# Performance work log

Hardware: AMD Instinct MI355X
Metric: run time of the kernel (lower is better)

## Reference

```python
import jax, jax.numpy as jnp
import numpy as np

L = 512      # number of grid points
B = 32768    # batch of independent trajectories


def _rhs(y, w):
    # y: [4, B] -> dy: [4, B]; tiny coupled polynomial vector field
    A, T, N, C = y
    dA = w[0] + w[1] * A + w[2] * A ** 2
    dT = w[3] + w[4] * T + w[5] * T ** 2 + w[6] * A + w[7] * A ** 2 + w[8] * A * T
    dN = w[9] + w[10] * N + w[11] * N ** 2 + w[12] * T + w[13] * T ** 2 + w[14] * T * N
    dC = w[15] + w[16] * C + w[17] * C ** 2 + w[18] * N + w[19] * N ** 2 + w[20] * N * C
    return jnp.stack([dA, dT, dN, dC])


def setup_inputs() -> dict:
    key = jax.random.key(0)
    k1, k2 = jax.random.split(key)
    s_grid = jnp.arange(L, dtype=jnp.float32) * 0.01  # increasing grid, small h
    y0 = jax.random.normal(k1, (4, B), dtype=jnp.float32)
    w = jax.random.normal(k2, (21,), dtype=jnp.float32) * 0.001  # nn.Parameter init
    return {"s_grid": s_grid, "y0": y0, "w": w}


def reference(s_grid, y0, w):
    hs = jnp.diff(s_grid)  # [L-1] step sizes h_i = s[i] - s[i-1]

    def step(y, h):
        y_next = y + h * _rhs(y, w)  # explicit Euler
        return y_next, y_next

    _, ys = jax.lax.scan(step, y0, hs)          # [L-1, 4, B]
    return jnp.concatenate([y0[None], ys], 0)   # [L, 4, B]
```

## Files before the change

### kernel.cpp

```cpp
#include <hip/hip_runtime.h>


#define ODE_L 512
#define ODE_B 32768
#define G     8

#define ODE_STEP(h)                                                          \
  do {                                                                       \
    const float dA = w0  + w1  * A + w2  * A * A;                            \
    const float dT = w3  + w4  * T + w5  * T * T + w6  * A + w7  * A * A +   \
                     w8  * A * T;                                            \
    const float dN = w9  + w10 * N + w11 * N * N + w12 * T + w13 * T * T +   \
                     w14 * T * N;                                            \
    const float dC = w15 + w16 * C + w17 * C * C + w18 * N + w19 * N * N +   \
                     w20 * N * C;                                            \
    A += h * dA; T += h * dT; N += h * dN; C += h * dC;                      \
  } while (0)

#define ODE_GROUP(OFS, R0V)                                                  \
  do {                                                                       \
    _Pragma("unroll")                                                        \
    for (int j = 0; j < G; ++j) {                                            \
      const float h = sh_h[(R0V) + j - 1];                                   \
      ODE_STEP(h);                                                           \
      bA[(OFS) + j] = A; bT[(OFS) + j] = T;                                  \
      bN[(OFS) + j] = N; bC[(OFS) + j] = C;                                  \
    }                                                                        \
    _Pragma("unroll")                                                        \
    for (int j = 0; j < G; ++j) {                                            \
      const unsigned o = ((R0V) + j) * (4u * ODE_B) + b;                     \
      out[o + 0u * ODE_B] = bA[(OFS) + j];                                   \
      out[o + 1u * ODE_B] = bT[(OFS) + j];                                   \
      out[o + 2u * ODE_B] = bN[(OFS) + j];                                   \
      out[o + 3u * ODE_B] = bC[(OFS) + j];                                   \
    }                                                                        \
  } while (0)

__global__ __launch_bounds__(64) void population_ode_kernel(
    const float* __restrict__ s_grid,
    const float* __restrict__ y0,
    const float* __restrict__ w,
    float* __restrict__ out)
{
    __shared__ float sh_h[ODE_L - 1];

    const int tid = threadIdx.x;
    #pragma unroll
    for (int i = tid; i < ODE_L - 1; i += 64) {
        sh_h[i] = s_grid[i + 1] - s_grid[i];
    }

    const float w0  = w[0],  w1  = w[1],  w2  = w[2];
    const float w3  = w[3],  w4  = w[4],  w5  = w[5],  w6  = w[6],  w7 = w[7],
                w8  = w[8];
    const float w9  = w[9],  w10 = w[10], w11 = w[11], w12 = w[12],
                w13 = w[13], w14 = w[14];
    const float w15 = w[15], w16 = w[16], w17 = w[17], w18 = w[18],
                w19 = w[19], w20 = w[20];

    __syncthreads();

    const unsigned b = blockIdx.x * 64u + (unsigned)tid;

    float A = y0[0 * ODE_B + b];
    float T = y0[1 * ODE_B + b];
    float N = y0[2 * ODE_B + b];
    float C = y0[3 * ODE_B + b];

    out[0u * ODE_B + b] = A;
    out[1u * ODE_B + b] = T;
    out[2u * ODE_B + b] = N;
    out[3u * ODE_B + b] = C;

    float bA[2 * G], bT[2 * G], bN[2 * G], bC[2 * G];

    for (unsigned g = 0; g < 31; ++g) {
        const unsigned r0 = 1u + g * (2 * G);
        ODE_GROUP(0, r0);
        ODE_GROUP(G, r0 + G);
    }

    ODE_GROUP(0, 497u);

    #pragma unroll
    for (int j = 0; j < 7; ++j) {
        const float h = sh_h[504 + j];
        ODE_STEP(h);
        bA[G + j] = A; bT[G + j] = T; bN[G + j] = N; bC[G + j] = C;
    }
    #pragma unroll
    for (int j = 0; j < 7; ++j) {
        const unsigned o = (505u + j) * (4u * ODE_B) + b;
        out[o + 0u * ODE_B] = bA[G + j];
        out[o + 1u * ODE_B] = bT[G + j];
        out[o + 2u * ODE_B] = bN[G + j];
        out[o + 3u * ODE_B] = bC[G + j];
    }
}

extern "C" void kernel_launch(void* const* d_in, const int* in_sizes, int n_in,
                              void* d_out, int out_size, void* d_ws, size_t ws_size,
                              hipStream_t stream) {
    (void)in_sizes; (void)n_in; (void)d_ws; (void)ws_size; (void)out_size;

    const float* s_grid = (const float*)d_in[0];
    const float* y0     = (const float*)d_in[1];
    const float* w      = (const float*)d_in[2];
    float* out          = (float*)d_out;

    population_ode_kernel<<<dim3(ODE_B / 64), dim3(64), 0, stream>>>(
        s_grid, y0, w, out);
}
```

Measured before the change: 265.0 us.

## Warp-specialize: one compute wave feeds four store waves via double-buffered LDS

Splits each block into a compute wave that integrates the Euler steps and four store waves, each writing one state component, with results exchanged through a double-buffered LDS buffer and barriers per group of steps. The aim is to overlap the serial ODE arithmetic with the global output stores and increase memory-level parallelism. The trade-offs are a block-wide barrier every eight steps and larger blocks.

```diff
diff --git a/kernel.cpp b/kernel.cpp
--- a/kernel.cpp
+++ b/kernel.cpp
@@ -4,6 +4,8 @@
 #define ODE_L 512
 #define ODE_B 32768
 #define G     8
+#define NGRP  64
+#define TPB   320
 
 #define ODE_STEP(h)                                                          \
   do {                                                                       \
@@ -17,36 +19,25 @@
     A += h * dA; T += h * dT; N += h * dN; C += h * dC;                      \
   } while (0)
 
-#define ODE_GROUP(OFS, R0V)                                                  \
-  do {                                                                       \
-    _Pragma("unroll")                                                        \
-    for (int j = 0; j < G; ++j) {                                            \
-      const float h = sh_h[(R0V) + j - 1];                                   \
-      ODE_STEP(h);                                                           \
-      bA[(OFS) + j] = A; bT[(OFS) + j] = T;                                  \
-      bN[(OFS) + j] = N; bC[(OFS) + j] = C;                                  \
-    }                                                                        \
-    _Pragma("unroll")                                                        \
-    for (int j = 0; j < G; ++j) {                                            \
-      const unsigned o = ((R0V) + j) * (4u * ODE_B) + b;                     \
-      out[o + 0u * ODE_B] = bA[(OFS) + j];                                   \
-      out[o + 1u * ODE_B] = bT[(OFS) + j];                                   \
-      out[o + 2u * ODE_B] = bN[(OFS) + j];                                   \
-      out[o + 3u * ODE_B] = bC[(OFS) + j];                                   \
-    }                                                                        \
-  } while (0)
+__device__ __forceinline__ void sync_lds() {
+    asm volatile("s_waitcnt lgkmcnt(0)" ::: "memory");
+    __builtin_amdgcn_s_barrier();
+}
 
-__global__ __launch_bounds__(64) void population_ode_kernel(
+__global__ __launch_bounds__(TPB) void population_ode_kernel(
     const float* __restrict__ s_grid,
     const float* __restrict__ y0,
     const float* __restrict__ w,
     float* __restrict__ out)
 {
     __shared__ float sh_h[ODE_L - 1];
+    __shared__ float buf[2][G][4][64];
 
-    const int tid = threadIdx.x;
-    #pragma unroll
-    for (int i = tid; i < ODE_L - 1; i += 64) {
+    const int tid  = threadIdx.x;
+    const int wid  = tid >> 6;
+    const int lane = tid & 63;
+
+    for (int i = tid; i < ODE_L - 1; i += TPB) {
         sh_h[i] = s_grid[i + 1] - s_grid[i];
     }
 
@@ -58,43 +49,61 @@
     const float w15 = w[15], w16 = w[16], w17 = w[17], w18 = w[18],
                 w19 = w[19], w20 = w[20];
 
-    __syncthreads();
+    const unsigned b = blockIdx.x * 64u + (unsigned)lane;
 
-    const unsigned b = blockIdx.x * 64u + (unsigned)tid;
+    sync_lds();
 
-    float A = y0[0 * ODE_B + b];
-    float T = y0[1 * ODE_B + b];
-    float N = y0[2 * ODE_B + b];
-    float C = y0[3 * ODE_B + b];
+    if (wid == 0) {
+        float A = y0[0 * ODE_B + b];
+        float T = y0[1 * ODE_B + b];
+        float N = y0[2 * ODE_B + b];
+        float C = y0[3 * ODE_B + b];
 
-    out[0u * ODE_B + b] = A;
-    out[1u * ODE_B + b] = T;
-    out[2u * ODE_B + b] = N;
-    out[3u * ODE_B + b] = C;
+        for (unsigned g = 0; g < NGRP - 1; ++g) {
+            const int p = (int)(g & 1u);
+            #pragma unroll
+            for (int j = 0; j < G; ++j) {
+                const float h = sh_h[g * G + j];
+                ODE_STEP(h);
+                buf[p][j][0][lane] = A;
+                buf[p][j][1][lane] = T;
+                buf[p][j][2][lane] = N;
+                buf[p][j][3][lane] = C;
+            }
+            sync_lds();
+        }
+        #pragma unroll
+        for (int j = 0; j < 7; ++j) {
+            const float h = sh_h[504 + j];
+            ODE_STEP(h);
+            buf[1][j][0][lane] = A;
+            buf[1][j][1][lane] = T;
+            buf[1][j][2][lane] = N;
+            buf[1][j][3][lane] = C;
+        }
+        sync_lds();
+    } else {
+        const int st = wid - 1;
+        const unsigned ob = (unsigned)st * ODE_B + b;
 
-    float bA[2 * G], bT[2 * G], bN[2 * G], bC[2 * G];
+        out[ob] = y0[ob];
+        sync_lds();
 
-    for (unsigned g = 0; g < 31; ++g) {
-        const unsigned r0 = 1u + g * (2 * G);
-        ODE_GROUP(0, r0);
-        ODE_GROUP(G, r0 + G);
-    }
-
-    ODE_GROUP(0, 497u);
-
-    #pragma unroll
-    for (int j = 0; j < 7; ++j) {
-        const float h = sh_h[504 + j];
-        ODE_STEP(h);
-        bA[G + j] = A; bT[G + j] = T; bN[G + j] = N; bC[G + j] = C;
-    }
-    #pragma unroll
-    for (int j = 0; j < 7; ++j) {
-        const unsigned o = (505u + j) * (4u * ODE_B) + b;
-        out[o + 0u * ODE_B] = bA[G + j];
-        out[o + 1u * ODE_B] = bT[G + j];
-        out[o + 2u * ODE_B] = bN[G + j];
-        out[o + 3u * ODE_B] = bC[G + j];
+        for (unsigned g = 1; g < NGRP; ++g) {
+            const int p = (int)((g - 1u) & 1u);
+            const unsigned r0 = 1u + (g - 1u) * G;
+            #pragma unroll
+            for (int j = 0; j < G; ++j) {
+                const float v = buf[p][j][st][lane];
+                out[(r0 + (unsigned)j) * (4u * ODE_B) + ob] = v;
+            }
+            sync_lds();
+        }
+        #pragma unroll
+        for (int j = 0; j < 7; ++j) {
+            const float v = buf[1][j][st][lane];
+            out[(505u + (unsigned)j) * (4u * ODE_B) + ob] = v;
+        }
     }
 }
 
@@ -108,6 +117,6 @@
     const float* w      = (const float*)d_in[2];
     float* out          = (float*)d_out;
 
-    population_ode_kernel<<<dim3(ODE_B / 64), dim3(64), 0, stream>>>(
+    population_ode_kernel<<<dim3(ODE_B / 64), dim3(TPB), 0, stream>>>(
         s_grid, y0, w, out);
 }
```

Result: no change. 266.8 us (+0.7%).
